# Kernel optimization log

Hardware: AMD Instinct MI355X
Metric: run time of the kernel (lower is better)

The kernel has to match this reference:

```python
import jax, jax.numpy as jnp
import numpy as np

GROUPS = 32
EPS = 1e-5


def setup_inputs() -> dict:
    key = jax.random.key(0)
    ks = jax.random.split(key, 3)
    B, C, H, W, D = 2, 512, 32, 32, 32
    x = jax.random.normal(ks[0], (B, C, H, W, D), dtype=jnp.float32)
    # 1x1 Conv3d weights squeezed to 2-D matrices; fan-in scaled init
    qkv_w = jax.random.normal(ks[1], (3 * C, C), dtype=jnp.float32) / np.sqrt(C)
    qkv_b = jnp.zeros((3 * C,), dtype=jnp.float32)
    proj_w = jax.random.normal(ks[2], (C, C), dtype=jnp.float32) / np.sqrt(C)
    proj_b = jnp.zeros((C,), dtype=jnp.float32)
    gn_w = jnp.ones((C,), dtype=jnp.float32)
    gn_b = jnp.zeros((C,), dtype=jnp.float32)
    return {"x": x, "gn_w": gn_w, "gn_b": gn_b, "qkv_w": qkv_w,
            "qkv_b": qkv_b, "proj_w": proj_w, "proj_b": proj_b}


def _group_norm(x, w, b):
    B, C = x.shape[0], x.shape[1]
    xg = x.reshape(B, GROUPS, C // GROUPS, -1)  # [B, G, C/G, N]
    mean = xg.mean(axis=(2, 3), keepdims=True)
    var = xg.var(axis=(2, 3), keepdims=True)
    xn = ((xg - mean) * jax.lax.rsqrt(var + EPS)).reshape(x.shape)
    shape = (1, C) + (1,) * (x.ndim - 2)
    return xn * w.reshape(shape) + b.reshape(shape)


def reference(x, gn_w, gn_b, qkv_w, qkv_b, proj_w, proj_b):
    B, C, H, W, D = x.shape
    N = H * W * D
    xn = _group_norm(x, gn_w, gn_b)
    xf = xn.reshape(B, C, N)
    # 1x1 conv3d == channel-mixing matmul over flattened spatial tokens
    qkv = jnp.einsum('oc,bcn->bon', qkv_w, xf) + qkv_b[None, :, None]
    q, k, v = jnp.split(qkv, 3, axis=1)  # each [B, C, N]
    scale = 1.0 / (C ** 0.5)
    # NOTE: faithful to source -- attention matrix is [B, C, C] (channel attention)
    attn = jax.nn.softmax(jnp.einsum('bcn,bdn->bcd', q, k) * scale, axis=-1)
    out = jnp.einsum('bcd,bdn->bcn', attn, v)  # [B, C, N]
    proj = jnp.einsum('oc,bcn->bon', proj_w, out) + proj_b[None, :, None]
    return x + proj.reshape(B, C, H, W, D)
```

## Files before the change

kernel.cpp:

```cpp
#include <hip/hip_runtime.h>
#include <cstdint>


typedef unsigned short u16;
typedef unsigned int u32;
typedef __bf16 bf16x8 __attribute__((ext_vector_type(8)));
typedef float f4 __attribute__((ext_vector_type(4)));

#define N_SP 32768
#define C_CH 512
#define NB 2
#define KSPLIT 32
#define LSTR 40

__device__ __forceinline__ float b2f(u16 h){
  union { float f; u32 u; } v; v.u = ((u32)h) << 16; return v.f;
}
__device__ __forceinline__ u16 f2b(float f){
  union { float f; u32 u; } v; v.f = f;
  u32 u = v.u;
  return (u16)((u + 0x7fffu + ((u >> 16) & 1u)) >> 16);
}
__device__ __forceinline__ void split(float v, u16& h, u16& l){
  h = f2b(v);
  l = f2b(v - b2f(h));
}

__global__ __launch_bounds__(256) void k_stats(const float* __restrict__ x,
                                               float* __restrict__ cs, float* __restrict__ cq){
  const long bc = blockIdx.x;
  const float* p = x + bc * (long)N_SP;
  const int t = threadIdx.x;
  float s = 0.f, q = 0.f;
  for(int i=0;i<32;i++){
    float4 v = *(const float4*)(p + i*1024 + t*4);
    s += v.x + v.y + v.z + v.w;
    q += v.x*v.x + v.y*v.y + v.z*v.z + v.w*v.w;
  }
  for(int off=32; off; off>>=1){ s += __shfl_down(s, off, 64); q += __shfl_down(q, off, 64); }
  __shared__ float rs[4], rq[4];
  int lane = t & 63, wv = t >> 6;
  if(lane==0){ rs[wv]=s; rq[wv]=q; }
  __syncthreads();
  if(t==0){ cs[bc] = rs[0]+rs[1]+rs[2]+rs[3]; cq[bc] = rq[0]+rq[1]+rq[2]+rq[3]; }
}

__global__ void k_gn(const float* __restrict__ cs, const float* __restrict__ cq,
                     const float* __restrict__ gw, const float* __restrict__ gb,
                     float* __restrict__ s_, float* __restrict__ t_, float* __restrict__ rxn){
  int i = blockIdx.x*blockDim.x + threadIdx.x;
  if(i >= NB*C_CH) return;
  int b = i >> 9, c = i & 511, g = c >> 4;
  int base = (b << 9) | (g << 4);
  float sum=0.f, sq=0.f;
  for(int j=0;j<16;j++){ sum += cs[base+j]; sq += cq[base+j]; }
  const float inv = 1.0f / (16.0f * (float)N_SP);
  float mean = sum * inv;
  float var = sq * inv - mean*mean;
  if(var < 0.f) var = 0.f;
  float rs = rsqrtf(var + 1e-5f);
  float sc = gw[c] * rs;
  float tt = gb[c] - mean * sc;
  s_[i] = sc; t_[i] = tt;
  rxn[i] = sc * cs[i] + (float)N_SP * tt;
}

__global__ __launch_bounds__(256) void k_gram(const float* __restrict__ x, float* __restrict__ Gp){
  __shared__ u16 Ah[128*LSTR], Al[128*LSTR], Bh[128*LSTR], Bl[128*LSTR];
  const int t = threadIdx.x;
  const int tile = blockIdx.x;
  const int ti = tile >> 2, tj = tile & 3;
  const int b = blockIdx.z;
  const int i0 = ti << 7, j0 = tj << 7;
  const long xb = (long)b * C_CH * (long)N_SP;
  const int k0 = blockIdx.y * (N_SP / KSPLIT);
  const int lane = t & 63, wave = t >> 6;
  const int wm = wave >> 1, wn = wave & 1;
  const int lr = lane & 15, quad = lane >> 4;
  const int srow = t >> 1, skh = (t & 1) << 4;

  f4 acc[4][4];
  for(int i=0;i<4;i++) for(int j=0;j<4;j++){ f4 z = {0.f,0.f,0.f,0.f}; acc[i][j]=z; }

  const float* gi = x + xb + (long)(i0 + srow)*N_SP + k0 + skh;
  const float* gj = x + xb + (long)(j0 + srow)*N_SP + k0 + skh;

  for(int kk=0; kk<N_SP/KSPLIT; kk+=32){
    float4 va[4], vb[4];
    #pragma unroll
    for(int j2=0;j2<4;j2++){ va[j2] = *(const float4*)(gi + kk + j2*4); vb[j2] = *(const float4*)(gj + kk + j2*4); }
    __syncthreads();
    #pragma unroll
    for(int j2=0;j2<4;j2++){
      float fa[4] = {va[j2].x, va[j2].y, va[j2].z, va[j2].w};
      float fb[4] = {vb[j2].x, vb[j2].y, vb[j2].z, vb[j2].w};
      u16 ha[4], la[4], hb[4], lb[4];
      #pragma unroll
      for(int e=0;e<4;e++){ split(fa[e], ha[e], la[e]); split(fb[e], hb[e], lb[e]); }
      int o = srow*LSTR + skh + j2*4;
      *(uint2*)&Ah[o] = *(uint2*)ha; *(uint2*)&Al[o] = *(uint2*)la;
      *(uint2*)&Bh[o] = *(uint2*)hb; *(uint2*)&Bl[o] = *(uint2*)lb;
    }
    __syncthreads();
    bf16x8 ah[4], al[4], bh[4], bl[4];
    #pragma unroll
    for(int mt=0; mt<4; mt++){
      int o = (wm*64 + mt*16 + lr)*LSTR + quad*8;
      ah[mt] = *(const bf16x8*)&Ah[o]; al[mt] = *(const bf16x8*)&Al[o];
    }
    #pragma unroll
    for(int nt=0; nt<4; nt++){
      int o = (wn*64 + nt*16 + lr)*LSTR + quad*8;
      bh[nt] = *(const bf16x8*)&Bh[o]; bl[nt] = *(const bf16x8*)&Bl[o];
    }
    #pragma unroll
    for(int mt=0; mt<4; mt++)
      #pragma unroll
      for(int nt=0; nt<4; nt++){
        acc[mt][nt] = __builtin_amdgcn_mfma_f32_16x16x32_bf16(ah[mt], bh[nt], acc[mt][nt], 0, 0, 0);
        acc[mt][nt] = __builtin_amdgcn_mfma_f32_16x16x32_bf16(ah[mt], bl[nt], acc[mt][nt], 0, 0, 0);
        acc[mt][nt] = __builtin_amdgcn_mfma_f32_16x16x32_bf16(al[mt], bh[nt], acc[mt][nt], 0, 0, 0);
      }
  }
  float* dst = Gp + ((long)(b*16 + tile)*KSPLIT + blockIdx.y) * 16384;
  #pragma unroll
  for(int mt=0; mt<4; mt++){
    #pragma unroll
    for(int nt=0; nt<4; nt++){
      int m = wm*64 + mt*16 + quad*4;
      int n = wn*64 + nt*16 + lr;
      #pragma unroll
      for(int r=0;r<4;r++)
        dst[(m + r)*128 + n] = acc[mt][nt][r];
    }
  }
}

__global__ __launch_bounds__(256) void k_G(const float* __restrict__ Gp, const float* __restrict__ s_,
                                           const float* __restrict__ t_, const float* __restrict__ cs,
                                           float* __restrict__ G){
  long idx4 = ((long)blockIdx.x*256 + threadIdx.x) * 4;
  int j = (int)(idx4 & 511);
  int i = (int)((idx4 >> 9) & 511);
  int b = (int)(idx4 >> 18);
  int tile = ((i >> 7) << 2) | (j >> 7);
  int il = i & 127, jl = j & 127;
  const float* src = Gp + ((long)(b*16 + tile)*KSPLIT) * 16384 + il*128 + jl;
  float ax=0.f, ay=0.f, az=0.f, aw=0.f;
  #pragma unroll 4
  for(int ks=0; ks<KSPLIT; ks++){
    float4 v = *(const float4*)(src + (long)ks*16384);
    ax += v.x; ay += v.y; az += v.z; aw += v.w;
  }
  long bo = (long)b << 9;
  float si = s_[bo+i], tii = t_[bo+i], csi = cs[bo+i];
  float g[4] = {ax, ay, az, aw};
  float4 out;
  float* po = (float*)&out;
  #pragma unroll
  for(int e=0;e<4;e++){
    int je = j + e;
    float sj = s_[bo+je], tj = t_[bo+je], csj = cs[bo+je];
    po[e] = si*sj*g[e] + si*csi*tj + tii*sj*csj + (float)N_SP*tii*tj;
  }
  *(float4*)&G[idx4] = out;
}

__global__ __launch_bounds__(256) void k_mm_nn(const float* __restrict__ A, long sA,
                                               const float* __restrict__ B, long sB,
                                               float* __restrict__ C, long sC){
  __shared__ float As_[16][68];
  __shared__ float Bs_[16][68];
  const int b = blockIdx.z;
  A += (long)b*sA; B += (long)b*sB; C += (long)b*sC;
  const int m0 = (blockIdx.x >> 3) << 6;
  const int n0 = (blockIdx.x & 7) << 6;
  const int t = threadIdx.x;
  const int tm = t >> 4, tn = t & 15;
  float acc[4][4] = {};
  const int ar = t >> 2, ac = (t & 3) << 2;
  const int br = t >> 4, bc = (t & 15) << 2;
  for(int k0=0; k0<512; k0+=16){
    float4 av = *(const float4*)&A[(long)(m0 + ar)*512 + k0 + ac];
    float4 bv = *(const float4*)&B[(long)(k0 + br)*512 + n0 + bc];
    __syncthreads();
    As_[ac+0][ar] = av.x; As_[ac+1][ar] = av.y; As_[ac+2][ar] = av.z; As_[ac+3][ar] = av.w;
    *(float4*)&Bs_[br][bc] = bv;
    __syncthreads();
    #pragma unroll
    for(int k=0;k<16;k++){
      float4 a4 = *(const float4*)&As_[k][tm<<2];
      float4 b4 = *(const float4*)&Bs_[k][tn<<2];
      float aa[4] = {a4.x,a4.y,a4.z,a4.w}, bb[4] = {b4.x,b4.y,b4.z,b4.w};
      #pragma unroll
      for(int i=0;i<4;i++)
        #pragma unroll
        for(int j=0;j<4;j++) acc[i][j] += aa[i]*bb[j];
    }
  }
  for(int i=0;i<4;i++) for(int j=0;j<4;j++)
    C[(long)(m0 + (tm<<2) + i)*512 + n0 + (tn<<2) + j] = acc[i][j];
}

__global__ __launch_bounds__(256) void k_mm_nt_logits(const float* __restrict__ A, long sA,
    const float* __restrict__ Bn, float* __restrict__ C, long sC,
    const float* __restrict__ aq, const float* __restrict__ ak,
    const float* __restrict__ bq, const float* __restrict__ bk, float scale){
  __shared__ float As_[16][68];
  __shared__ float Bs_[16][68];
  const int b = blockIdx.z;
  A += (long)b*sA; C += (long)b*sC;
  const float* aqb = aq + (long)b*512;
  const float* akb = ak + (long)b*512;
  const int m0 = (blockIdx.x >> 3) << 6;
  const int n0 = (blockIdx.x & 7) << 6;
  const int t = threadIdx.x;
  const int tm = t >> 4, tn = t & 15;
  float acc[4][4] = {};
  const int ar = t >> 2, ac = (t & 3) << 2;
  for(int k0=0; k0<512; k0+=16){
    float4 av = *(const float4*)&A[(long)(m0 + ar)*512 + k0 + ac];
    float4 bv = *(const float4*)&Bn[(long)(n0 + ar)*512 + k0 + ac];
    __syncthreads();
    As_[ac+0][ar] = av.x; As_[ac+1][ar] = av.y; As_[ac+2][ar] = av.z; As_[ac+3][ar] = av.w;
    Bs_[ac+0][ar] = bv.x; Bs_[ac+1][ar] = bv.y; Bs_[ac+2][ar] = bv.z; Bs_[ac+3][ar] = bv.w;
    __syncthreads();
    #pragma unroll
    for(int k=0;k<16;k++){
      float4 a4 = *(const float4*)&As_[k][tm<<2];
      float4 b4 = *(const float4*)&Bs_[k][tn<<2];
      float aa[4] = {a4.x,a4.y,a4.z,a4.w}, bb[4] = {b4.x,b4.y,b4.z,b4.w};
      #pragma unroll
      for(int i=0;i<4;i++)
        #pragma unroll
        for(int j=0;j<4;j++) acc[i][j] += aa[i]*bb[j];
    }
  }
  for(int i=0;i<4;i++) for(int j=0;j<4;j++){
    int gi = m0 + (tm<<2) + i, gj = n0 + (tn<<2) + j;
    float vv = acc[i][j] + aqb[gi]*bk[gj] + bq[gi]*(akb[gj] + (float)N_SP*bk[gj]);
    C[(long)gi*512 + gj] = scale*vv;
  }
}

__global__ __launch_bounds__(256) void k_softmax(float* __restrict__ L){
  const long row = blockIdx.x;
  float* p = L + row*512;
  const int t = threadIdx.x;
  float v0 = p[t], v1 = p[t+256];
  float m = fmaxf(v0, v1);
  for(int off=32; off; off>>=1) m = fmaxf(m, __shfl_down(m, off, 64));
  __shared__ float red[4], red2[4];
  int lane = t & 63, wv = t >> 6;
  if(lane==0) red[wv] = m;
  __syncthreads();
  float M = fmaxf(fmaxf(red[0],red[1]), fmaxf(red[2],red[3]));
  float e0 = __expf(v0 - M), e1 = __expf(v1 - M);
  float s = e0 + e1;
  for(int off=32; off; off>>=1) s += __shfl_down(s, off, 64);
  if(lane==0) red2[wv] = s;
  __syncthreads();
  float inv = 1.0f / (red2[0]+red2[1]+red2[2]+red2[3]);
  p[t] = e0*inv; p[t+256] = e1*inv;
}

__global__ __launch_bounds__(128) void k_rowdot(const float* __restrict__ M, long sM,
    const float* __restrict__ v, long sv, float* __restrict__ out, long sout,
    const float* __restrict__ addv, long saddv, int accum){
  const int i = blockIdx.x, b = blockIdx.y;
  const float* Mr = M + (long)b*sM + (long)i*512;
  const float* vb = v + (long)b*sv;
  const int t = threadIdx.x;
  float s = Mr[t]*vb[t] + Mr[t+128]*vb[t+128] + Mr[t+256]*vb[t+256] + Mr[t+384]*vb[t+384];
  for(int off=32; off; off>>=1) s += __shfl_down(s, off, 64);
  __shared__ float r2[2];
  if((t&63)==0) r2[t>>6] = s;
  __syncthreads();
  if(t==0){
    float r = r2[0] + r2[1];
    long oi = (long)b*sout + i;
    if(addv) r += addv[(long)b*saddv + i];
    if(accum) r += out[oi];
    out[oi] = r;
  }
}

__global__ void k_af(const float* __restrict__ A, const float* __restrict__ s_,
                     u16* __restrict__ Afh, u16* __restrict__ Afl){
  long idx = (long)blockIdx.x*256 + threadIdx.x;
  int k = idx & 511; long b = idx >> 18;
  float vv = A[idx] * s_[(b<<9) + k];
  u16 h, l; split(vv, h, l);
  Afh[idx] = h; Afl[idx] = l;
}

__global__ __launch_bounds__(256) void k_final(const u16* __restrict__ Afh, const u16* __restrict__ Afl,
                                               const float* __restrict__ x, const float* __restrict__ cf,
                                               float* __restrict__ y){
  __shared__ u16 Ah[128*LSTR], Al[128*LSTR], Bh[128*LSTR], Bl[128*LSTR];
  const int t = threadIdx.x;
  const int b = blockIdx.z;
  const int n0 = blockIdx.x << 7;
  const int m0 = blockIdx.y << 7;
  const int lane = t & 63, wave = t >> 6;
  const int wm = wave >> 1, wn = wave & 1;
  const int lr = lane & 15, quad = lane >> 4;
  const int arow = t >> 1, akh = (t & 1) << 4;
  const long afb = (long)b*C_CH*C_CH;
  const int kp = (t & 15) << 1;
  const int nq = (t >> 4) << 3;
  const long xb = (long)b*C_CH*(long)N_SP;

  f4 acc[4][4];
  for(int i=0;i<4;i++) for(int j=0;j<4;j++){ f4 z = {0.f,0.f,0.f,0.f}; acc[i][j]=z; }

  for(int kk=0; kk<C_CH; kk+=32){
    const u16* gah = Afh + afb + (long)(m0 + arow)*C_CH + kk + akh;
    const u16* gal = Afl + afb + (long)(m0 + arow)*C_CH + kk + akh;
    uint4 vah0 = *(const uint4*)(gah);
    uint4 vah1 = *(const uint4*)(gah + 8);
    uint4 val0 = *(const uint4*)(gal);
    uint4 val1 = *(const uint4*)(gal + 8);
    const float* gx0 = x + xb + (long)(kk + kp)*N_SP + n0 + nq;
    float4 vx00 = *(const float4*)(gx0);
    float4 vx01 = *(const float4*)(gx0 + 4);
    float4 vx10 = *(const float4*)(gx0 + N_SP);
    float4 vx11 = *(const float4*)(gx0 + N_SP + 4);
    __syncthreads();
    int ao = arow*LSTR + akh;
    *(uint4*)&Ah[ao] = vah0; *(uint4*)&Ah[ao+8] = vah1;
    *(uint4*)&Al[ao] = val0; *(uint4*)&Al[ao+8] = val1;
    float f0[8] = {vx00.x,vx00.y,vx00.z,vx00.w, vx01.x,vx01.y,vx01.z,vx01.w};
    float f1[8] = {vx10.x,vx10.y,vx10.z,vx10.w, vx11.x,vx11.y,vx11.z,vx11.w};
    #pragma unroll
    for(int j=0;j<8;j++){
      u16 h0,l0,h1,l1;
      split(f0[j], h0, l0); split(f1[j], h1, l1);
      int o = (nq + j)*LSTR + kp;
      *(u32*)&Bh[o] = (u32)h0 | ((u32)h1 << 16);
      *(u32*)&Bl[o] = (u32)l0 | ((u32)l1 << 16);
    }
    __syncthreads();
    bf16x8 ah[4], al[4], bh[4], bl[4];
    #pragma unroll
    for(int mt=0; mt<4; mt++){
      int o = (wm*64 + mt*16 + lr)*LSTR + quad*8;
      ah[mt] = *(const bf16x8*)&Ah[o]; al[mt] = *(const bf16x8*)&Al[o];
    }
    #pragma unroll
    for(int nt=0; nt<4; nt++){
      int o = (wn*64 + nt*16 + lr)*LSTR + quad*8;
      bh[nt] = *(const bf16x8*)&Bh[o]; bl[nt] = *(const bf16x8*)&Bl[o];
    }
    #pragma unroll
    for(int mt=0; mt<4; mt++)
      #pragma unroll
      for(int nt=0; nt<4; nt++){
        acc[mt][nt] = __builtin_amdgcn_mfma_f32_16x16x32_bf16(ah[mt], bh[nt], acc[mt][nt], 0, 0, 0);
        acc[mt][nt] = __builtin_amdgcn_mfma_f32_16x16x32_bf16(ah[mt], bl[nt], acc[mt][nt], 0, 0, 0);
        acc[mt][nt] = __builtin_amdgcn_mfma_f32_16x16x32_bf16(al[mt], bh[nt], acc[mt][nt], 0, 0, 0);
      }
  }
  #pragma unroll
  for(int mt=0; mt<4; mt++){
    int mbase = m0 + wm*64 + mt*16 + quad*4;
    float cfv[4];
    #pragma unroll
    for(int r=0;r<4;r++) cfv[r] = cf[b*C_CH + mbase + r];
    #pragma unroll
    for(int nt=0; nt<4; nt++){
      int n = n0 + wn*64 + nt*16 + lr;
      #pragma unroll
      for(int r=0;r<4;r++){
        long idx = xb + (long)(mbase + r)*N_SP + n;
        y[idx] = acc[mt][nt][r] + x[idx] + cfv[r];
      }
    }
  }
}

extern "C" void kernel_launch(void* const* d_in, const int* in_sizes, int n_in,
                              void* d_out, int out_size, void* d_ws, size_t ws_size,
                              hipStream_t stream){
  const float* x    = (const float*)d_in[0];
  const float* gnw  = (const float*)d_in[1];
  const float* gnb  = (const float*)d_in[2];
  const float* qkvw = (const float*)d_in[3];
  const float* qkvb = (const float*)d_in[4];
  const float* pw   = (const float*)d_in[5];
  const float* pb   = (const float*)d_in[6];
  float* y = (float*)d_out;

  char* w = (char*)d_out;
  size_t off = 0;
  auto alloc = [&](size_t bytes)->void*{
    void* p = w + off; off = (off + bytes + 255) & ~(size_t)255; return p;
  };
  float* GP   = (float*)alloc((size_t)NB*16*KSPLIT*16384*4);
  float* G    = (float*)alloc((size_t)NB*C_CH*C_CH*4);
  float* T1   = (float*)alloc((size_t)NB*C_CH*C_CH*4);
  float* ATT  = (float*)alloc((size_t)NB*C_CH*C_CH*4);
  float* M0   = (float*)alloc((size_t)NB*C_CH*C_CH*4);
  float* AM   = (float*)alloc((size_t)NB*C_CH*C_CH*4);

  char* w2 = (char*)d_ws;
  size_t off2 = 0;
  auto alloc2 = [&](size_t bytes)->void*{
    void* p = w2 + off2; off2 = (off2 + bytes + 255) & ~(size_t)255; return p;
  };
  u16*   AFH  = (u16*)  alloc2((size_t)NB*C_CH*C_CH*2);
  u16*   AFL  = (u16*)  alloc2((size_t)NB*C_CH*C_CH*2);
  float* CF   = (float*)alloc2(NB*C_CH*4);
  float* CS   = (float*)alloc2(NB*C_CH*4);
  float* CQ   = (float*)alloc2(NB*C_CH*4);
  float* S_   = (float*)alloc2(NB*C_CH*4);
  float* T_   = (float*)alloc2(NB*C_CH*4);
  float* RXN  = (float*)alloc2(NB*C_CH*4);
  float* AQ   = (float*)alloc2(NB*C_CH*4);
  float* AK   = (float*)alloc2(NB*C_CH*4);
  float* E    = (float*)alloc2(NB*C_CH*4);
  (void)ws_size; (void)in_sizes; (void)n_in; (void)out_size;

  const float scale = 0.04419417382415922f;

  k_stats<<<NB*C_CH, 256, 0, stream>>>(x, CS, CQ);
  k_gn<<<4, 256, 0, stream>>>(CS, CQ, gnw, gnb, S_, T_, RXN);
  k_gram<<<dim3(16, KSPLIT, NB), 256, 0, stream>>>(x, GP);
  k_G<<<512, 256, 0, stream>>>(GP, S_, T_, CS, G);
  k_mm_nn<<<dim3(64,1,NB), 256, 0, stream>>>(qkvw, 0, G, 262144, T1, 262144);
  k_rowdot<<<dim3(512,NB), 128, 0, stream>>>(qkvw,          0, RXN, 512, AQ, 512, nullptr, 0, 0);
  k_rowdot<<<dim3(512,NB), 128, 0, stream>>>(qkvw+262144,   0, RXN, 512, AK, 512, nullptr, 0, 0);
  k_mm_nt_logits<<<dim3(64,1,NB), 256, 0, stream>>>(T1, 262144, qkvw+262144, ATT, 262144,
                                                    AQ, AK, qkvb, qkvb+512, scale);
  k_softmax<<<NB*C_CH, 256, 0, stream>>>(ATT);
  k_rowdot<<<dim3(512,NB), 128, 0, stream>>>(ATT, 262144, qkvb+1024, 0, E, 512, nullptr, 0, 0);
  k_mm_nn<<<dim3(64,1,NB), 256, 0, stream>>>(ATT, 262144, qkvw+524288, 0, M0, 262144);
  k_mm_nn<<<dim3(64,1,NB), 256, 0, stream>>>(pw, 0, M0, 262144, AM, 262144);
  k_rowdot<<<dim3(512,NB), 128, 0, stream>>>(AM, 262144, T_, 512, CF, 512, nullptr, 0, 0);
  k_rowdot<<<dim3(512,NB), 128, 0, stream>>>(pw, 0, E, 512, CF, 512, pb, 0, 1);
  k_af<<<(NB*C_CH*C_CH)/256, 256, 0, stream>>>(AM, S_, AFH, AFL);
  k_final<<<dim3(N_SP/128, C_CH/128, NB), 256, 0, stream>>>(AFH, AFL, x, CF, y);
}
```

Before: 647.6 us.

## Prefetch next k-slice in gram and final GEMMs; load A fragments directly from global

In the gram kernel, global loads for the next k-step are issued right after the LDS store barrier, so they overlap with the MFMA work, and a trailing barrier protects the LDS buffers. In the final GEMM the tile changes to 256x64, with each wave owning 64 rows. The A (hi/lo bf16) fragments are read straight from global/L2 instead of staged through LDS, and the x tile is register-prefetched one step ahead. This cuts LDS traffic and barrier stalls at the cost of uncoalesced-ish direct global A loads and more B tiles per row.

```diff
diff --git a/kernel.cpp b/kernel.cpp
--- a/kernel.cpp
+++ b/kernel.cpp
@@ -85,11 +85,11 @@
   const float* gi = x + xb + (long)(i0 + srow)*N_SP + k0 + skh;
   const float* gj = x + xb + (long)(j0 + srow)*N_SP + k0 + skh;
 
+  float4 va[4], vb[4];
+  #pragma unroll
+  for(int j2=0;j2<4;j2++){ va[j2] = *(const float4*)(gi + j2*4); vb[j2] = *(const float4*)(gj + j2*4); }
+
   for(int kk=0; kk<N_SP/KSPLIT; kk+=32){
-    float4 va[4], vb[4];
-    #pragma unroll
-    for(int j2=0;j2<4;j2++){ va[j2] = *(const float4*)(gi + kk + j2*4); vb[j2] = *(const float4*)(gj + kk + j2*4); }
-    __syncthreads();
     #pragma unroll
     for(int j2=0;j2<4;j2++){
       float fa[4] = {va[j2].x, va[j2].y, va[j2].z, va[j2].w};
@@ -102,6 +102,13 @@
       *(uint2*)&Bh[o] = *(uint2*)hb; *(uint2*)&Bl[o] = *(uint2*)lb;
     }
     __syncthreads();
+    if(kk + 32 < N_SP/KSPLIT){
+      #pragma unroll
+      for(int j2=0;j2<4;j2++){
+        va[j2] = *(const float4*)(gi + kk + 32 + j2*4);
+        vb[j2] = *(const float4*)(gj + kk + 32 + j2*4);
+      }
+    }
     bf16x8 ah[4], al[4], bh[4], bl[4];
     #pragma unroll
     for(int mt=0; mt<4; mt++){
@@ -121,6 +128,7 @@
         acc[mt][nt] = __builtin_amdgcn_mfma_f32_16x16x32_bf16(ah[mt], bl[nt], acc[mt][nt], 0, 0, 0);
         acc[mt][nt] = __builtin_amdgcn_mfma_f32_16x16x32_bf16(al[mt], bh[nt], acc[mt][nt], 0, 0, 0);
       }
+    __syncthreads();
   }
   float* dst = Gp + ((long)(b*16 + tile)*KSPLIT + blockIdx.y) * 16384;
   #pragma unroll
@@ -297,43 +305,31 @@
 __global__ __launch_bounds__(256) void k_final(const u16* __restrict__ Afh, const u16* __restrict__ Afl,
                                                const float* __restrict__ x, const float* __restrict__ cf,
                                                float* __restrict__ y){
-  __shared__ u16 Ah[128*LSTR], Al[128*LSTR], Bh[128*LSTR], Bl[128*LSTR];
+  __shared__ u16 Bh[64*LSTR], Bl[64*LSTR];
   const int t = threadIdx.x;
   const int b = blockIdx.z;
-  const int n0 = blockIdx.x << 7;
-  const int m0 = blockIdx.y << 7;
+  const int n0 = blockIdx.x << 6;
+  const int m0 = blockIdx.y << 8;
   const int lane = t & 63, wave = t >> 6;
-  const int wm = wave >> 1, wn = wave & 1;
   const int lr = lane & 15, quad = lane >> 4;
-  const int arow = t >> 1, akh = (t & 1) << 4;
+  const int mw = m0 + (wave << 6);
+  const int kp = (t & 15) << 1;
+  const int nq = (t >> 4) << 2;
+  const long xb = (long)b*C_CH*(long)N_SP;
   const long afb = (long)b*C_CH*C_CH;
-  const int kp = (t & 15) << 1;
-  const int nq = (t >> 4) << 3;
-  const long xb = (long)b*C_CH*(long)N_SP;
 
   f4 acc[4][4];
   for(int i=0;i<4;i++) for(int j=0;j<4;j++){ f4 z = {0.f,0.f,0.f,0.f}; acc[i][j]=z; }
 
+  const float* gx0 = x + xb + (long)kp*N_SP + n0 + nq;
+  float4 vx0 = *(const float4*)(gx0);
+  float4 vx1 = *(const float4*)(gx0 + N_SP);
+
   for(int kk=0; kk<C_CH; kk+=32){
-    const u16* gah = Afh + afb + (long)(m0 + arow)*C_CH + kk + akh;
-    const u16* gal = Afl + afb + (long)(m0 + arow)*C_CH + kk + akh;
-    uint4 vah0 = *(const uint4*)(gah);
-    uint4 vah1 = *(const uint4*)(gah + 8);
-    uint4 val0 = *(const uint4*)(gal);
-    uint4 val1 = *(const uint4*)(gal + 8);
-    const float* gx0 = x + xb + (long)(kk + kp)*N_SP + n0 + nq;
-    float4 vx00 = *(const float4*)(gx0);
-    float4 vx01 = *(const float4*)(gx0 + 4);
-    float4 vx10 = *(const float4*)(gx0 + N_SP);
-    float4 vx11 = *(const float4*)(gx0 + N_SP + 4);
-    __syncthreads();
-    int ao = arow*LSTR + akh;
-    *(uint4*)&Ah[ao] = vah0; *(uint4*)&Ah[ao+8] = vah1;
-    *(uint4*)&Al[ao] = val0; *(uint4*)&Al[ao+8] = val1;
-    float f0[8] = {vx00.x,vx00.y,vx00.z,vx00.w, vx01.x,vx01.y,vx01.z,vx01.w};
-    float f1[8] = {vx10.x,vx10.y,vx10.z,vx10.w, vx11.x,vx11.y,vx11.z,vx11.w};
-    #pragma unroll
-    for(int j=0;j<8;j++){
+    float f0[4] = {vx0.x, vx0.y, vx0.z, vx0.w};
+    float f1[4] = {vx1.x, vx1.y, vx1.z, vx1.w};
+    #pragma unroll
+    for(int j=0;j<4;j++){
       u16 h0,l0,h1,l1;
       split(f0[j], h0, l0); split(f1[j], h1, l1);
       int o = (nq + j)*LSTR + kp;
@@ -341,15 +337,23 @@
       *(u32*)&Bl[o] = (u32)l0 | ((u32)l1 << 16);
     }
     __syncthreads();
-    bf16x8 ah[4], al[4], bh[4], bl[4];
+    bf16x8 ah[4], al[4];
+    const u16* gah = Afh + afb + (long)(mw + lr)*C_CH + kk + quad*8;
+    const u16* gal = Afl + afb + (long)(mw + lr)*C_CH + kk + quad*8;
     #pragma unroll
     for(int mt=0; mt<4; mt++){
-      int o = (wm*64 + mt*16 + lr)*LSTR + quad*8;
-      ah[mt] = *(const bf16x8*)&Ah[o]; al[mt] = *(const bf16x8*)&Al[o];
-    }
+      ah[mt] = *(const bf16x8*)(gah + mt*16*C_CH);
+      al[mt] = *(const bf16x8*)(gal + mt*16*C_CH);
+    }
+    if(kk + 32 < C_CH){
+      const float* gxn = x + xb + (long)(kk + 32 + kp)*N_SP + n0 + nq;
+      vx0 = *(const float4*)(gxn);
+      vx1 = *(const float4*)(gxn + N_SP);
+    }
+    bf16x8 bh[4], bl[4];
     #pragma unroll
     for(int nt=0; nt<4; nt++){
-      int o = (wn*64 + nt*16 + lr)*LSTR + quad*8;
+      int o = (nt*16 + lr)*LSTR + quad*8;
       bh[nt] = *(const bf16x8*)&Bh[o]; bl[nt] = *(const bf16x8*)&Bl[o];
     }
     #pragma unroll
@@ -360,16 +364,17 @@
         acc[mt][nt] = __builtin_amdgcn_mfma_f32_16x16x32_bf16(ah[mt], bl[nt], acc[mt][nt], 0, 0, 0);
         acc[mt][nt] = __builtin_amdgcn_mfma_f32_16x16x32_bf16(al[mt], bh[nt], acc[mt][nt], 0, 0, 0);
       }
+    __syncthreads();
   }
   #pragma unroll
   for(int mt=0; mt<4; mt++){
-    int mbase = m0 + wm*64 + mt*16 + quad*4;
+    int mbase = mw + mt*16 + quad*4;
     float cfv[4];
     #pragma unroll
     for(int r=0;r<4;r++) cfv[r] = cf[b*C_CH + mbase + r];
     #pragma unroll
     for(int nt=0; nt<4; nt++){
-      int n = n0 + wn*64 + nt*16 + lr;
+      int n = n0 + nt*16 + lr;
       #pragma unroll
       for(int r=0;r<4;r++){
         long idx = xb + (long)(mbase + r)*N_SP + n;
@@ -439,5 +444,5 @@
   k_rowdot<<<dim3(512,NB), 128, 0, stream>>>(AM, 262144, T_, 512, CF, 512, nullptr, 0, 0);
   k_rowdot<<<dim3(512,NB), 128, 0, stream>>>(pw, 0, E, 512, CF, 512, pb, 0, 1);
   k_af<<<(NB*C_CH*C_CH)/256, 256, 0, stream>>>(AM, S_, AFH, AFL);
-  k_final<<<dim3(N_SP/128, C_CH/128, NB), 256, 0, stream>>>(AFH, AFL, x, CF, y);
-}
+  k_final<<<dim3(N_SP/64, 2, NB), 256, 0, stream>>>(AFH, AFL, x, CF, y);
+}
```

Result: slower. 673.5 us (+4.0%).
